# Performance work log

Measured on AMD Instinct MI355X. Metric: run time of the kernel, lower is better.

The kernel has to match this reference:

```python
import jax, jax.numpy as jnp
import numpy as np

N_NODES = 100000
N_EDGES = 1600000
IN_CH = 128
HID = 128
OUT_CH = 2
NUM_GRAPHS = 512


def _mlp_params(key, d_in, d_out):
    k1, k2 = jax.random.split(key)
    s1 = 1.0 / np.sqrt(d_in)
    s2 = 1.0 / np.sqrt(d_out)
    return (jax.random.uniform(k1, (d_in, d_out), jnp.float32, -s1, s1),
            jnp.zeros((d_out,), jnp.float32),
            jax.random.uniform(k2, (d_out, d_out), jnp.float32, -s2, s2),
            jnp.zeros((d_out,), jnp.float32))


def setup_inputs() -> dict:
    key = jax.random.key(0)
    ks = jax.random.split(key, 8)
    x = jax.random.normal(ks[0], (N_NODES, IN_CH), jnp.float32)
    edge_index = jax.random.randint(ks[1], (2, N_EDGES), 0, N_NODES, jnp.int64)
    batch = jnp.sort(jax.random.randint(ks[2], (N_NODES,), 0, NUM_GRAPHS, jnp.int64))
    w1_0, b1_0, w2_0, b2_0 = _mlp_params(ks[3], IN_CH, HID)
    w1_1, b1_1, w2_1, b2_1 = _mlp_params(ks[4], HID, HID)
    w1_2, b1_2, w2_2, b2_2 = _mlp_params(ks[5], HID, HID)
    s = 1.0 / np.sqrt(HID)
    w_lin = jax.random.uniform(ks[6], (HID, OUT_CH), jnp.float32, -s, s)
    b_lin = jnp.zeros((OUT_CH,), jnp.float32)
    return {"x": x, "edge_index": edge_index, "batch": batch,
            "w1_0": w1_0, "b1_0": b1_0, "w2_0": w2_0, "b2_0": b2_0,
            "w1_1": w1_1, "b1_1": b1_1, "w2_1": w2_1, "b2_1": b2_1,
            "w1_2": w1_2, "b1_2": b1_2, "w2_2": w2_2, "b2_2": b2_2,
            "w_lin": w_lin, "b_lin": b_lin}


def _gin_conv(x, src, dst, w1, b1, w2, b2):
    # GINConv with eps=0: MLP(x + sum_{j in N(i)} x_j)
    agg = jax.ops.segment_sum(x[src], dst, num_segments=N_NODES)  # [N, d]
    h = x + agg
    h = jax.nn.relu(h @ w1 + b1)
    return h @ w2 + b2


def reference(x, edge_index, batch,
              w1_0, b1_0, w2_0, b2_0,
              w1_1, b1_1, w2_1, b2_1,
              w1_2, b1_2, w2_2, b2_2,
              w_lin, b_lin):
    src, dst = edge_index[0], edge_index[1]
    h = _gin_conv(x, src, dst, w1_0, b1_0, w2_0, b2_0)
    h = jax.nn.relu(h)
    h = jax.nn.relu(_gin_conv(h, src, dst, w1_1, b1_1, w2_1, b2_1))
    h = jax.nn.relu(h)  # forward applies relu twice after GIN1
    h = _gin_conv(h, src, dst, w1_2, b1_2, w2_2, b2_2)
    # global mean pool per graph
    sums = jax.ops.segment_sum(h, batch, num_segments=NUM_GRAPHS)  # [G, d]
    counts = jax.ops.segment_sum(jnp.ones((N_NODES,), h.dtype), batch,
                                 num_segments=NUM_GRAPHS)
    pooled = sums / jnp.maximum(counts, 1.0)[:, None]
    # dropout is identity in eval mode
    return pooled @ w_lin + b_lin  # [G, OUT_CH]
```

## Files before the change

### kernel.cpp

```cpp
#include <hip/hip_runtime.h>
#include <hip/hip_bf16.h>

#define N_NODES   100000
#define N_EDGES   1600000
#define IN_CH     128
#define HID       128
#define OUT_CH    2
#define NUM_GRAPHS 512

#define BKT_SHIFT 9
#define NB2 ((N_NODES + 511) >> BKT_SHIFT)
#define PB  200
#define CHUNK (N_EDGES / PB)

#define NCAST (N_NODES * IN_CH / 4 / 256)

typedef __attribute__((ext_vector_type(8))) short bf16x8;
typedef __attribute__((ext_vector_type(4))) float f32x4;
typedef unsigned int uint32;
typedef unsigned long long uint64;

static __device__ __forceinline__ float b2f(uint32 b) {
    return __uint_as_float(b << 16);
}
static __device__ __forceinline__ unsigned short f2b(float f) {
    uint32 u = __float_as_uint(f);
    u += 0x7fffu + ((u >> 16) & 1u);
    return (unsigned short)(u >> 16);
}
static __device__ __forceinline__ void acc8(float* a, int4 v) {
    uint32 x;
    x = (uint32)v.x; a[0] += __uint_as_float(x << 16); a[1] += __uint_as_float(x & 0xffff0000u);
    x = (uint32)v.y; a[2] += __uint_as_float(x << 16); a[3] += __uint_as_float(x & 0xffff0000u);
    x = (uint32)v.z; a[4] += __uint_as_float(x << 16); a[5] += __uint_as_float(x & 0xffff0000u);
    x = (uint32)v.w; a[6] += __uint_as_float(x << 16); a[7] += __uint_as_float(x & 0xffff0000u);
}

__global__ void k_front(const float* __restrict__ x, unsigned short* __restrict__ h,
                        const float* w0, const float* w1, const float* w2,
                        const float* w3, const float* w4, const float* w5,
                        unsigned short* __restrict__ wt,
                        const int* __restrict__ dst, int* __restrict__ histG) {
    __shared__ int hist[NB2];
    int bid = blockIdx.x, t = threadIdx.x;
    if (bid < NCAST) {
        int base = (bid * 256 + t) * 4;
        float4 v = *(const float4*)(x + base);
        ushort4 o;
        o.x = f2b(v.x); o.y = f2b(v.y); o.z = f2b(v.z); o.w = f2b(v.w);
        *(ushort4*)(h + base) = o;
    } else if (bid < NCAST + 6) {
        const float* ws[6] = {w0, w1, w2, w3, w4, w5};
        int wi = bid - NCAST;
        const float* w = ws[wi];
        unsigned short* o = wt + wi * 16384;
        for (int i = t; i < 16384; i += 256) {
            int k = i >> 7, n = i & 127;
            o[n * 128 + k] = f2b(w[i]);
        }
    } else {
        int blk = bid - NCAST - 6;
        for (int i = t; i < NB2; i += 256) hist[i] = 0;
        __syncthreads();
        int base = blk * CHUNK;
        for (int i = t; i < CHUNK; i += 256)
            atomicAdd(&hist[dst[base + i] >> BKT_SHIFT], 1);
        __syncthreads();
        for (int i = t; i < NB2; i += 256) histG[i * PB + blk] = hist[i];
    }
}

__global__ void k_scan1(const int* __restrict__ in, int* __restrict__ out,
                        int* __restrict__ bsum, int n) {
    __shared__ int sm[256];
    int b = blockIdx.x, t = threadIdx.x;
    int base = b * 1024 + t * 4;
    int v0 = 0, v1 = 0, v2 = 0, v3 = 0;
    if (base + 3 < n) {
        int4 q = *(const int4*)(in + base);
        v0 = q.x; v1 = q.y; v2 = q.z; v3 = q.w;
    } else {
        if (base + 0 < n) v0 = in[base + 0];
        if (base + 1 < n) v1 = in[base + 1];
        if (base + 2 < n) v2 = in[base + 2];
        if (base + 3 < n) v3 = in[base + 3];
    }
    int s = v0 + v1 + v2 + v3;
    sm[t] = s;
    __syncthreads();
    for (int off = 1; off < 256; off <<= 1) {
        int u = (t >= off) ? sm[t - off] : 0;
        __syncthreads();
        sm[t] += u;
        __syncthreads();
    }
    int p = (t == 0) ? 0 : sm[t - 1];
    int o0 = p, o1 = p + v0, o2 = o1 + v1, o3 = o2 + v2;
    if (base + 3 < n) {
        *(int4*)(out + base) = make_int4(o0, o1, o2, o3);
    } else {
        if (base + 0 < n) out[base + 0] = o0;
        if (base + 1 < n) out[base + 1] = o1;
        if (base + 2 < n) out[base + 2] = o2;
        if (base + 3 < n) out[base + 3] = o3;
    }
    if (t == 255) bsum[b] = s + ((t == 0) ? 0 : sm[t - 1]);
}

__global__ void k_scan3b(int* __restrict__ out, const int* __restrict__ bsum, int n) {
    __shared__ int add_s;
    int b = blockIdx.x, t = threadIdx.x;
    if (t == 0) {
        int s = 0;
        for (int i = 0; i < b; ++i) s += bsum[i];
        add_s = s;
    }
    __syncthreads();
    int add = add_s;
    int base = b * 1024 + t * 4;
    if (base + 3 < n) {
        int4 q = *(const int4*)(out + base);
        q.x += add; q.y += add; q.z += add; q.w += add;
        *(int4*)(out + base) = q;
    } else {
        for (int j = 0; j < 4; ++j)
            if (base + j < n) out[base + j] += add;
    }
}

__global__ void k_p3g(const int* __restrict__ ei, const int* __restrict__ baseG,
                      uint64* __restrict__ ebuf,
                      const int* __restrict__ batch, int* __restrict__ goff) {
    __shared__ int cur[NB2];
    int t = threadIdx.x, blk = blockIdx.x;
    if (blk >= PB) {
        int g = (blk - PB) * 512 + t;
        if (g <= NUM_GRAPHS) {
            int lo = 0, hi = N_NODES;
            while (lo < hi) {
                int mid = (lo + hi) >> 1;
                if (batch[mid] < g) lo = mid + 1; else hi = mid;
            }
            goff[g] = lo;
        }
        return;
    }
    for (int i = t; i < NB2; i += 512) cur[i] = baseG[i * PB + blk];
    __syncthreads();
    int base = blk * CHUNK;
    for (int i = t; i < CHUNK; i += 512) {
        int e = base + i;
        int src = ei[e];
        int dst = ei[N_EDGES + e];
        int pos = atomicAdd(&cur[dst >> BKT_SHIFT], 1);
        ebuf[pos] = ((uint64)(uint32)dst << 32) | (uint32)src;
    }
}

__global__ void k_p4(const uint64* __restrict__ ebuf, const int* __restrict__ baseG,
                     int* __restrict__ off, int* __restrict__ csr) {
    __shared__ int ldeg[512];
    __shared__ int lscan[512];
    __shared__ int lcur[512];
    int b = blockIdx.x, t = threadIdx.x;
    int node0 = b << BKT_SHIFT;
    int nn = min(512, N_NODES - node0);
    int e0 = baseG[b * PB];
    int e1 = (b == NB2 - 1) ? N_EDGES : baseG[(b + 1) * PB];
    ldeg[t] = 0;
    __syncthreads();
    for (int e = e0 + t; e < e1; e += 512) {
        int dst = (int)(ebuf[e] >> 32);
        atomicAdd(&ldeg[dst - node0], 1);
    }
    __syncthreads();
    lscan[t] = ldeg[t];
    __syncthreads();
    for (int o = 1; o < 512; o <<= 1) {
        int v = (t >= o) ? lscan[t - o] : 0;
        __syncthreads();
        lscan[t] += v;
        __syncthreads();
    }
    int excl = (t == 0) ? 0 : lscan[t - 1];
    lcur[t] = e0 + excl;
    if (t < nn) off[node0 + t] = e0 + excl;
    if (b == NB2 - 1 && t == 0) off[N_NODES] = N_EDGES;
    __syncthreads();
    for (int e = e0 + t; e < e1; e += 512) {
        uint64 pr = ebuf[e];
        int dst = (int)(pr >> 32);
        int pos = atomicAdd(&lcur[dst - node0], 1);
        csr[pos] = (int)(pr & 0xffffffffu);
    }
}

__global__ void k_agg(const unsigned short* __restrict__ h,
                      const int* __restrict__ off, const int* __restrict__ csr,
                      unsigned short* __restrict__ hs) {
    int wid = (blockIdx.x * 256 + threadIdx.x) >> 6;
    int lane = threadIdx.x & 63;
    if (wid >= N_NODES) return;
    int g = lane >> 4, sub = lane & 15;
    int e0 = off[wid], e1 = off[wid + 1];
    float a[8] = {0.f, 0.f, 0.f, 0.f, 0.f, 0.f, 0.f, 0.f};
    int e = e0 + g;
    if (e + 12 < e1) {
        int s0 = csr[e], s1 = csr[e + 4], s2 = csr[e + 8], s3 = csr[e + 12];
        e += 16;
        while (e + 12 < e1) {
            int t0 = csr[e], t1 = csr[e + 4], t2 = csr[e + 8], t3 = csr[e + 12];
            int4 v0 = *(const int4*)(h + (size_t)s0 * 128 + sub * 8);
            int4 v1 = *(const int4*)(h + (size_t)s1 * 128 + sub * 8);
            int4 v2 = *(const int4*)(h + (size_t)s2 * 128 + sub * 8);
            int4 v3 = *(const int4*)(h + (size_t)s3 * 128 + sub * 8);
            acc8(a, v0); acc8(a, v1); acc8(a, v2); acc8(a, v3);
            s0 = t0; s1 = t1; s2 = t2; s3 = t3;
            e += 16;
        }
        int4 v0 = *(const int4*)(h + (size_t)s0 * 128 + sub * 8);
        int4 v1 = *(const int4*)(h + (size_t)s1 * 128 + sub * 8);
        int4 v2 = *(const int4*)(h + (size_t)s2 * 128 + sub * 8);
        int4 v3 = *(const int4*)(h + (size_t)s3 * 128 + sub * 8);
        acc8(a, v0); acc8(a, v1); acc8(a, v2); acc8(a, v3);
    }
    for (; e + 4 < e1; e += 8) {
        int s0 = csr[e];
        int s1 = csr[e + 4];
        int4 v0 = *(const int4*)(h + (size_t)s0 * 128 + sub * 8);
        int4 v1 = *(const int4*)(h + (size_t)s1 * 128 + sub * 8);
        acc8(a, v0);
        acc8(a, v1);
    }
    if (e < e1) {
        int s0 = csr[e];
        int4 v0 = *(const int4*)(h + (size_t)s0 * 128 + sub * 8);
        acc8(a, v0);
    }
#pragma unroll
    for (int j = 0; j < 8; ++j) {
        a[j] += __shfl_xor(a[j], 16);
        a[j] += __shfl_xor(a[j], 32);
    }
    if (g == 0) {
        int4 sv = *(const int4*)(h + (size_t)wid * 128 + sub * 8);
        acc8(a, sv);
        int4 o;
        o.x = (int)((uint32)f2b(a[0]) | ((uint32)f2b(a[1]) << 16));
        o.y = (int)((uint32)f2b(a[2]) | ((uint32)f2b(a[3]) << 16));
        o.z = (int)((uint32)f2b(a[4]) | ((uint32)f2b(a[5]) << 16));
        o.w = (int)((uint32)f2b(a[6]) | ((uint32)f2b(a[7]) << 16));
        *(int4*)(hs + (size_t)wid * 128 + sub * 8) = o;
    }
}

template<int OUTER_RELU>
__global__ void k_mlp(const unsigned short* __restrict__ hs,
                      const unsigned short* __restrict__ w1t, const float* __restrict__ b1,
                      const unsigned short* __restrict__ w2t, const float* __restrict__ b2,
                      unsigned short* __restrict__ ho) {
    __shared__ unsigned short T[64 * 128];
    int tid = threadIdx.x;
    int lane = tid & 63, wave = tid >> 6;
    int l15 = lane & 15, l4 = lane >> 4;
    int row0 = blockIdx.x * 64;
    int wn0 = wave * 32;

    bf16x8 w1f[2][4], w2f[2][4];
#pragma unroll
    for (int nt = 0; nt < 2; ++nt)
#pragma unroll
        for (int k = 0; k < 4; ++k) {
            int o = (wn0 + nt * 16 + l15) * 128 + k * 32 + l4 * 8;
            w1f[nt][k] = *(const bf16x8*)(w1t + o);
            w2f[nt][k] = *(const bf16x8*)(w2t + o);
        }
    float bias1[2] = { b1[wn0 + l15], b1[wn0 + 16 + l15] };
    float bias2[2] = { b2[wn0 + l15], b2[wn0 + 16 + l15] };

#pragma unroll
    for (int mt = 0; mt < 4; ++mt) {
        int arow = row0 + mt * 16 + l15;
        if (arow >= N_NODES) arow = N_NODES - 1;
        const unsigned short* ap = hs + (size_t)arow * 128 + l4 * 8;
        bf16x8 a0 = *(const bf16x8*)(ap);
        bf16x8 a1 = *(const bf16x8*)(ap + 32);
        bf16x8 a2 = *(const bf16x8*)(ap + 64);
        bf16x8 a3 = *(const bf16x8*)(ap + 96);
#pragma unroll
        for (int nt = 0; nt < 2; ++nt) {
            f32x4 acc = {0.f, 0.f, 0.f, 0.f};
            acc = __builtin_amdgcn_mfma_f32_16x16x32_bf16(a0, w1f[nt][0], acc, 0, 0, 0);
            acc = __builtin_amdgcn_mfma_f32_16x16x32_bf16(a1, w1f[nt][1], acc, 0, 0, 0);
            acc = __builtin_amdgcn_mfma_f32_16x16x32_bf16(a2, w1f[nt][2], acc, 0, 0, 0);
            acc = __builtin_amdgcn_mfma_f32_16x16x32_bf16(a3, w1f[nt][3], acc, 0, 0, 0);
#pragma unroll
            for (int j = 0; j < 4; ++j) {
                float v = fmaxf(acc[j] + bias1[nt], 0.f);
                int trow = mt * 16 + l4 * 4 + j;
                int tcol = wn0 + nt * 16 + l15;
                int byte = (trow * 256 + tcol * 2) ^ ((trow & 7) << 4);
                *(unsigned short*)((char*)T + byte) = f2b(v);
            }
        }
    }
    __syncthreads();

#pragma unroll
    for (int mt = 0; mt < 4; ++mt) {
        int trow = mt * 16 + l15;
        int sw = (trow & 7) << 4;
        int rb = trow * 256 + l4 * 16;
        bf16x8 t0 = *(const bf16x8*)((const char*)T + ((rb + 0)   ^ sw));
        bf16x8 t1 = *(const bf16x8*)((const char*)T + ((rb + 64)  ^ sw));
        bf16x8 t2 = *(const bf16x8*)((const char*)T + ((rb + 128) ^ sw));
        bf16x8 t3 = *(const bf16x8*)((const char*)T + ((rb + 192) ^ sw));
        __syncthreads();
#pragma unroll
        for (int nt = 0; nt < 2; ++nt) {
            f32x4 acc = {0.f, 0.f, 0.f, 0.f};
            acc = __builtin_amdgcn_mfma_f32_16x16x32_bf16(t0, w2f[nt][0], acc, 0, 0, 0);
            acc = __builtin_amdgcn_mfma_f32_16x16x32_bf16(t1, w2f[nt][1], acc, 0, 0, 0);
            acc = __builtin_amdgcn_mfma_f32_16x16x32_bf16(t2, w2f[nt][2], acc, 0, 0, 0);
            acc = __builtin_amdgcn_mfma_f32_16x16x32_bf16(t3, w2f[nt][3], acc, 0, 0, 0);
#pragma unroll
            for (int j = 0; j < 4; ++j) {
                float v = acc[j] + bias2[nt];
                if (OUTER_RELU) v = fmaxf(v, 0.f);
                int orow = mt * 16 + l4 * 4 + j;
                int ocol = wn0 + nt * 16 + l15;
                int byte = (orow * 256 + ocol * 2) ^ ((orow & 7) << 4);
                *(unsigned short*)((char*)T + byte) = f2b(v);
            }
        }
    }
    __syncthreads();

    for (int c = tid; c < 1024; c += 256) {
        int r = c >> 4, cc = c & 15;
        int byte = (r * 256 + cc * 16) ^ ((r & 7) << 4);
        int4 v = *(const int4*)((const char*)T + byte);
        int gr = row0 + r;
        if (gr < N_NODES)
            *(int4*)(ho + (size_t)gr * 128 + cc * 8) = v;
    }
}

__global__ void k_pool(const unsigned short* __restrict__ h,
                       const int* __restrict__ goff,
                       const float* __restrict__ wl, const float* __restrict__ bl,
                       float* __restrict__ out) {
    int g = blockIdx.x;
    int lane = threadIdx.x;
    int e0 = goff[g], e1 = goff[g + 1];
    int c2 = lane << 1;
    float s0 = 0.f, s1 = 0.f;
    int r = e0;
    for (; r + 3 < e1; r += 4) {
        uint32 v0 = *(const uint32*)(h + (size_t)r * 128 + c2);
        uint32 v1 = *(const uint32*)(h + (size_t)(r + 1) * 128 + c2);
        uint32 v2 = *(const uint32*)(h + (size_t)(r + 2) * 128 + c2);
        uint32 v3 = *(const uint32*)(h + (size_t)(r + 3) * 128 + c2);
        s0 += b2f(v0 & 0xffffu) + b2f(v1 & 0xffffu) + b2f(v2 & 0xffffu) + b2f(v3 & 0xffffu);
        s1 += b2f(v0 >> 16) + b2f(v1 >> 16) + b2f(v2 >> 16) + b2f(v3 >> 16);
    }
    for (; r < e1; ++r) {
        uint32 v = *(const uint32*)(h + (size_t)r * 128 + c2);
        s0 += b2f(v & 0xffffu);
        s1 += b2f(v >> 16);
    }
    float inv = 1.f / fmaxf((float)(e1 - e0), 1.f);
    s0 *= inv; s1 *= inv;
    float o0 = s0 * wl[c2 * 2]     + s1 * wl[(c2 + 1) * 2];
    float o1 = s0 * wl[c2 * 2 + 1] + s1 * wl[(c2 + 1) * 2 + 1];
#pragma unroll
    for (int d = 32; d; d >>= 1) {
        o0 += __shfl_down(o0, d);
        o1 += __shfl_down(o1, d);
    }
    if (lane == 0) {
        out[g * 2]     = o0 + bl[0];
        out[g * 2 + 1] = o1 + bl[1];
    }
}

extern "C" void kernel_launch(void* const* d_in, const int* in_sizes, int n_in,
                              void* d_out, int out_size, void* d_ws, size_t ws_size,
                              hipStream_t stream) {
    const float* x     = (const float*)d_in[0];
    const int*   ei    = (const int*)d_in[1];
    const int*   batch = (const int*)d_in[2];
    const float* w1[3] = {(const float*)d_in[3],  (const float*)d_in[7],  (const float*)d_in[11]};
    const float* b1[3] = {(const float*)d_in[4],  (const float*)d_in[8],  (const float*)d_in[12]};
    const float* w2[3] = {(const float*)d_in[5],  (const float*)d_in[9],  (const float*)d_in[13]};
    const float* b2[3] = {(const float*)d_in[6],  (const float*)d_in[10], (const float*)d_in[14]};
    const float* wl    = (const float*)d_in[15];
    const float* bl    = (const float*)d_in[16];

    char* p = (char*)d_ws;
    auto alloc = [&](size_t bytes) {
        char* r = p;
        p += (bytes + 255) & ~(size_t)255;
        return r;
    };
    int* off    = (int*)alloc((size_t)(N_NODES + 1) * 4);
    int* goff   = (int*)alloc((size_t)(NUM_GRAPHS + 1) * 4);
    int* histG  = (int*)alloc((size_t)(NB2 * PB) * 4);
    int* baseG  = (int*)alloc((size_t)(NB2 * PB + 1) * 4);
    int* bsum   = (int*)alloc((size_t)128 * 4);
    int* csr    = (int*)alloc((size_t)N_EDGES * 4);
    unsigned short* wts = (unsigned short*)alloc((size_t)6 * 16384 * 2);
    unsigned short* hA  = (unsigned short*)alloc((size_t)N_NODES * 128 * 2);
    unsigned short* hS  = (unsigned short*)alloc((size_t)N_NODES * 128 * 2);
    unsigned short* hB  = (unsigned short*)alloc((size_t)N_NODES * 128 * 2);
    uint64* ebuf = (uint64*)hS;

    k_front<<<NCAST + 6 + PB, 256, 0, stream>>>(x, hA,
        w1[0], w2[0], w1[1], w2[1], w1[2], w2[2], wts, ei + N_EDGES, histG);

    const int SCAN_N = NB2 * PB;
    const int SCAN_BLOCKS = (SCAN_N + 1023) / 1024;
    k_scan1<<<SCAN_BLOCKS, 256, 0, stream>>>(histG, baseG, bsum, SCAN_N);
    k_scan3b<<<SCAN_BLOCKS, 256, 0, stream>>>(baseG, bsum, SCAN_N);
    k_p3g<<<PB + 2, 512, 0, stream>>>(ei, baseG, ebuf, batch, goff);
    k_p4<<<NB2, 512, 0, stream>>>(ebuf, baseG, off, csr);

    unsigned short* wt1[3] = {wts,             wts + 2 * 16384, wts + 4 * 16384};
    unsigned short* wt2[3] = {wts + 1 * 16384, wts + 3 * 16384, wts + 5 * 16384};

    const int AGG_GRID = N_NODES / 4;
    const int MLP_GRID = (N_NODES + 63) / 64;

    k_agg<<<AGG_GRID, 256, 0, stream>>>(hA, off, csr, hS);
    k_mlp<1><<<MLP_GRID, 256, 0, stream>>>(hS, wt1[0], b1[0], wt2[0], b2[0], hB);
    k_agg<<<AGG_GRID, 256, 0, stream>>>(hB, off, csr, hS);
    k_mlp<1><<<MLP_GRID, 256, 0, stream>>>(hS, wt1[1], b1[1], wt2[1], b2[1], hA);
    k_agg<<<AGG_GRID, 256, 0, stream>>>(hA, off, csr, hS);
    k_mlp<0><<<MLP_GRID, 256, 0, stream>>>(hS, wt1[2], b1[2], wt2[2], b2[2], hB);

    k_pool<<<NUM_GRAPHS, 64, 0, stream>>>(hB, goff, wl, bl, (float*)d_out);
}
```

Baseline: 362.3 us.

## Shrink MLP row tile, parallelize pooling across waves, simplify agg loop

Three unrelated changes. The MLP tile drops from 64 to 32 rows per block, which doubles the grid and halves shared memory, and the bounds checks are removed because N_NODES divides evenly by 32. The pooling kernel now uses four waves per graph with a shared-memory reduction instead of one wave, spreading the per-graph row loads. The aggregation loop's software-pipelined index prefetch is replaced by a plain loop, which may expose csr load latency.

```diff
diff --git a/kernel.cpp b/kernel.cpp
--- a/kernel.cpp
+++ b/kernel.cpp
@@ -205,19 +205,8 @@
     int e0 = off[wid], e1 = off[wid + 1];
     float a[8] = {0.f, 0.f, 0.f, 0.f, 0.f, 0.f, 0.f, 0.f};
     int e = e0 + g;
-    if (e + 12 < e1) {
+    for (; e + 12 < e1; e += 16) {
         int s0 = csr[e], s1 = csr[e + 4], s2 = csr[e + 8], s3 = csr[e + 12];
-        e += 16;
-        while (e + 12 < e1) {
-            int t0 = csr[e], t1 = csr[e + 4], t2 = csr[e + 8], t3 = csr[e + 12];
-            int4 v0 = *(const int4*)(h + (size_t)s0 * 128 + sub * 8);
-            int4 v1 = *(const int4*)(h + (size_t)s1 * 128 + sub * 8);
-            int4 v2 = *(const int4*)(h + (size_t)s2 * 128 + sub * 8);
-            int4 v3 = *(const int4*)(h + (size_t)s3 * 128 + sub * 8);
-            acc8(a, v0); acc8(a, v1); acc8(a, v2); acc8(a, v3);
-            s0 = t0; s1 = t1; s2 = t2; s3 = t3;
-            e += 16;
-        }
         int4 v0 = *(const int4*)(h + (size_t)s0 * 128 + sub * 8);
         int4 v1 = *(const int4*)(h + (size_t)s1 * 128 + sub * 8);
         int4 v2 = *(const int4*)(h + (size_t)s2 * 128 + sub * 8);
@@ -259,11 +248,11 @@
                       const unsigned short* __restrict__ w1t, const float* __restrict__ b1,
                       const unsigned short* __restrict__ w2t, const float* __restrict__ b2,
                       unsigned short* __restrict__ ho) {
-    __shared__ unsigned short T[64 * 128];
+    __shared__ unsigned short T[32 * 128];
     int tid = threadIdx.x;
     int lane = tid & 63, wave = tid >> 6;
     int l15 = lane & 15, l4 = lane >> 4;
-    int row0 = blockIdx.x * 64;
+    int row0 = blockIdx.x * 32;
     int wn0 = wave * 32;
 
     bf16x8 w1f[2][4], w2f[2][4];
@@ -279,9 +268,8 @@
     float bias2[2] = { b2[wn0 + l15], b2[wn0 + 16 + l15] };
 
 #pragma unroll
-    for (int mt = 0; mt < 4; ++mt) {
+    for (int mt = 0; mt < 2; ++mt) {
         int arow = row0 + mt * 16 + l15;
-        if (arow >= N_NODES) arow = N_NODES - 1;
         const unsigned short* ap = hs + (size_t)arow * 128 + l4 * 8;
         bf16x8 a0 = *(const bf16x8*)(ap);
         bf16x8 a1 = *(const bf16x8*)(ap + 32);
@@ -307,7 +295,7 @@
     __syncthreads();
 
 #pragma unroll
-    for (int mt = 0; mt < 4; ++mt) {
+    for (int mt = 0; mt < 2; ++mt) {
         int trow = mt * 16 + l15;
         int sw = (trow & 7) << 4;
         int rb = trow * 256 + l4 * 16;
@@ -336,13 +324,11 @@
     }
     __syncthreads();
 
-    for (int c = tid; c < 1024; c += 256) {
+    for (int c = tid; c < 512; c += 256) {
         int r = c >> 4, cc = c & 15;
         int byte = (r * 256 + cc * 16) ^ ((r & 7) << 4);
         int4 v = *(const int4*)((const char*)T + byte);
-        int gr = row0 + r;
-        if (gr < N_NODES)
-            *(int4*)(ho + (size_t)gr * 128 + cc * 8) = v;
+        *(int4*)(ho + (size_t)(row0 + r) * 128 + cc * 8) = v;
     }
 }
 
@@ -350,37 +336,44 @@
                        const int* __restrict__ goff,
                        const float* __restrict__ wl, const float* __restrict__ bl,
                        float* __restrict__ out) {
+    __shared__ float sm[4][64][2];
     int g = blockIdx.x;
-    int lane = threadIdx.x;
+    int tid = threadIdx.x;
+    int wave = tid >> 6, lane = tid & 63;
     int e0 = goff[g], e1 = goff[g + 1];
     int c2 = lane << 1;
     float s0 = 0.f, s1 = 0.f;
-    int r = e0;
-    for (; r + 3 < e1; r += 4) {
+    int r = e0 + wave;
+    for (; r + 4 < e1; r += 8) {
         uint32 v0 = *(const uint32*)(h + (size_t)r * 128 + c2);
-        uint32 v1 = *(const uint32*)(h + (size_t)(r + 1) * 128 + c2);
-        uint32 v2 = *(const uint32*)(h + (size_t)(r + 2) * 128 + c2);
-        uint32 v3 = *(const uint32*)(h + (size_t)(r + 3) * 128 + c2);
-        s0 += b2f(v0 & 0xffffu) + b2f(v1 & 0xffffu) + b2f(v2 & 0xffffu) + b2f(v3 & 0xffffu);
-        s1 += b2f(v0 >> 16) + b2f(v1 >> 16) + b2f(v2 >> 16) + b2f(v3 >> 16);
-    }
-    for (; r < e1; ++r) {
+        uint32 v1 = *(const uint32*)(h + (size_t)(r + 4) * 128 + c2);
+        s0 += b2f(v0 & 0xffffu) + b2f(v1 & 0xffffu);
+        s1 += b2f(v0 >> 16) + b2f(v1 >> 16);
+    }
+    if (r < e1) {
         uint32 v = *(const uint32*)(h + (size_t)r * 128 + c2);
         s0 += b2f(v & 0xffffu);
         s1 += b2f(v >> 16);
     }
-    float inv = 1.f / fmaxf((float)(e1 - e0), 1.f);
-    s0 *= inv; s1 *= inv;
-    float o0 = s0 * wl[c2 * 2]     + s1 * wl[(c2 + 1) * 2];
-    float o1 = s0 * wl[c2 * 2 + 1] + s1 * wl[(c2 + 1) * 2 + 1];
-#pragma unroll
-    for (int d = 32; d; d >>= 1) {
-        o0 += __shfl_down(o0, d);
-        o1 += __shfl_down(o1, d);
-    }
-    if (lane == 0) {
-        out[g * 2]     = o0 + bl[0];
-        out[g * 2 + 1] = o1 + bl[1];
+    sm[wave][lane][0] = s0;
+    sm[wave][lane][1] = s1;
+    __syncthreads();
+    if (wave == 0) {
+        s0 = sm[0][lane][0] + sm[1][lane][0] + sm[2][lane][0] + sm[3][lane][0];
+        s1 = sm[0][lane][1] + sm[1][lane][1] + sm[2][lane][1] + sm[3][lane][1];
+        float inv = 1.f / fmaxf((float)(e1 - e0), 1.f);
+        s0 *= inv; s1 *= inv;
+        float o0 = s0 * wl[c2 * 2]     + s1 * wl[(c2 + 1) * 2];
+        float o1 = s0 * wl[c2 * 2 + 1] + s1 * wl[(c2 + 1) * 2 + 1];
+#pragma unroll
+        for (int d = 32; d; d >>= 1) {
+            o0 += __shfl_down(o0, d);
+            o1 += __shfl_down(o1, d);
+        }
+        if (lane == 0) {
+            out[g * 2]     = o0 + bl[0];
+            out[g * 2 + 1] = o1 + bl[1];
+        }
     }
 }
 
@@ -429,7 +422,7 @@
     unsigned short* wt2[3] = {wts + 1 * 16384, wts + 3 * 16384, wts + 5 * 16384};
 
     const int AGG_GRID = N_NODES / 4;
-    const int MLP_GRID = (N_NODES + 63) / 64;
+    const int MLP_GRID = N_NODES / 32;
 
     k_agg<<<AGG_GRID, 256, 0, stream>>>(hA, off, csr, hS);
     k_mlp<1><<<MLP_GRID, 256, 0, stream>>>(hS, wt1[0], b1[0], wt2[0], b2[0], hB);
@@ -438,5 +431,5 @@
     k_agg<<<AGG_GRID, 256, 0, stream>>>(hA, off, csr, hS);
     k_mlp<0><<<MLP_GRID, 256, 0, stream>>>(hS, wt1[2], b1[2], wt2[2], b2[2], hB);
 
-    k_pool<<<NUM_GRAPHS, 64, 0, stream>>>(hB, goff, wl, bl, (float*)d_out);
-}
+    k_pool<<<NUM_GRAPHS, 256, 0, stream>>>(hB, goff, wl, bl, (float*)d_out);
+}
```

New measurement: 375.9 us. +3.8%, slower.
